# Kernel optimization log

Measured on AMD Instinct MI355X. Metric: run time of the kernel, lower is better.

## Reference

```python
import jax, jax.numpy as jnp
import numpy as np

FILTERS = [1, 3, 7, 9]
BN_EPS = 1e-5


def _conv1d(x, w, b):
    # x: [B, C, L], w: [O, I, F] (torch Conv1d layout), 'same' padding for odd F
    pad = (w.shape[-1] - 1) // 2
    y = jax.lax.conv_general_dilated(
        x, w, window_strides=(1,), padding=[(pad, pad)],
        dimension_numbers=("NCH", "OIH", "NCH"))
    return y + b[None, :, None]


def _bn_elu(x, gamma, beta):
    # BatchNorm1d in training mode: biased batch stats over (batch, length)
    m = jnp.mean(x, axis=(0, 2), keepdims=True)
    v = jnp.var(x, axis=(0, 2), keepdims=True)
    xn = (x - m) * jax.lax.rsqrt(v + BN_EPS)
    return jax.nn.elu(xn * gamma[None, :, None] + beta[None, :, None])


def setup_inputs() -> dict:
    key = jax.random.key(0)
    ks = jax.random.split(key, 32)
    b, h, l, lk, dk = 8, 8, 1024, 1024, 64
    inp = {
        "Q": jax.random.normal(ks[0], (b, h, l, dk), jnp.float32),
        "K": jax.random.normal(ks[1], (b, h, lk, dk), jnp.float32),
        "V": jax.random.normal(ks[2], (b, h, lk, dk), jnp.float32),
        "W_pq": jax.random.normal(ks[3], (1, dk), jnp.float32) * 0.1,
        "W_bq": jax.random.normal(ks[4], (dk, 1), jnp.float32) * 0.1,
        "W_bk": jax.random.normal(ks[5], (dk, 1), jnp.float32) * 0.1,
        "bn_g": jax.random.uniform(ks[6], (h,), jnp.float32, 0.5, 1.5),
        "bn_b": jax.random.normal(ks[7], (h,), jnp.float32) * 0.1,
        "attn_mask": jnp.ones((1,), dtype=bool),
    }
    for i, f in enumerate(FILTERS):
        s = 1.0 / np.sqrt(h * f)
        inp[f"cq_w{i}"] = jax.random.normal(ks[8 + i], (h, h, f), jnp.float32) * s
        inp[f"cq_b{i}"] = jax.random.normal(ks[12 + i], (h,), jnp.float32) * 0.05
        inp[f"ck_w{i}"] = jax.random.normal(ks[16 + i], (h, h, f), jnp.float32) * s
        inp[f"ck_b{i}"] = jax.random.normal(ks[20 + i], (h,), jnp.float32) * 0.05
    return inp


def reference(Q, K, V, W_pq, W_bq, W_bk,
              cq_w0, cq_b0, cq_w1, cq_b1, cq_w2, cq_b2, cq_w3, cq_b3,
              ck_w0, ck_b0, ck_w1, ck_b1, ck_w2, ck_b2, ck_w3, ck_b3,
              bn_g, bn_b, attn_mask):
    b, h, l, dk = Q.shape
    lk = K.shape[2]
    nf = len(FILTERS)
    # proj_q applied to BOTH Q and K (proj_k is dead in the original code)
    q = jnp.einsum("bhld,d->bhl", Q, W_pq[0])  # [b,h,l]
    k = jnp.einsum("bhld,d->bhl", K, W_pq[0])  # [b,h,lk]
    cq = [(cq_w0, cq_b0), (cq_w1, cq_b1), (cq_w2, cq_b2), (cq_w3, cq_b3)]
    ck = [(ck_w0, ck_b0), (ck_w1, ck_b1), (ck_w2, ck_b2), (ck_w3, ck_b3)]
    Q_l = [_bn_elu(_conv1d(q, w, bb), bn_g, bn_b) for w, bb in cq]
    K_l = [_bn_elu(_conv1d(k, w, bb), bn_g, bn_b) for w, bb in ck]
    # replicate torch.cat(dim=0) + reshape(b,h,nf*len) flat-order semantics
    Q_p = jnp.concatenate(Q_l, axis=0).reshape(b, h, nf * l)    # [b,h,4l]
    K_p = jnp.concatenate(K_l, axis=0).reshape(b, h, nf * lk)   # [b,h,4lk]
    Qt = jax.lax.top_k(Q_p, l)[0]                               # [b,h,l]
    Km = jnp.mean(K_p.reshape(b, h, nf, lk), axis=2)            # [b,h,lk]
    Kt = jax.lax.top_k(Km, lk)[0]                               # descending sort
    Qb = Qt[..., None] * W_bq[:, 0]                             # [b,h,l,dk]
    Kb = Kt[..., None] * W_bk[:, 0]                             # [b,h,lk,dk]
    scores = jnp.einsum("bhqd,bhkd->bhqk", Qb, Kb) / np.float32(np.sqrt(dk))
    attn = jax.nn.softmax(scores, axis=-1)
    context = jnp.einsum("bhqk,bhkd->bhqd", attn, V)
    return context, attn
```

## Files before the change

kernel.cpp:

```cpp
#include <hip/hip_runtime.h>
#include <hip/hip_bf16.h>
#include <math.h>

namespace {
constexpr int CONV_OFF = 131072;
constexpr int PS_OFF   = 655360;
constexpr int PSS_OFF  = 659456;

typedef short bf16x8 __attribute__((ext_vector_type(8)));
typedef float f32x4 __attribute__((ext_vector_type(4)));

union BF8 {
  bf16x8 v;
  short s[8];
};

__device__ inline float bn_elu(float v, float mean, float rstd, float g,
                               float be) {
  const float x = (v - mean) * rstd * g + be;
  return x > 0.f ? x : expm1f(x);
}

__device__ inline void cswap(float& a, float& b, bool up) {
  const float mx = fmaxf(a, b), mn = fminf(a, b);
  a = up ? mx : mn;
  b = up ? mn : mx;
}

__device__ inline void wsort1024(float v[16], int lane) {
#pragma unroll
  for (int k = 2; k <= 1024; k <<= 1) {
#pragma unroll
    for (int j = 512; j >= 16; j >>= 1) {
      if (j <= (k >> 1)) {
        const int lj = j >> 4;
        const bool up = ((lane & (k >> 4)) == 0);
        const bool keep = (up == ((lane & lj) == 0));
#pragma unroll
        for (int e = 0; e < 16; ++e) {
          const float p = __shfl_xor(v[e], lj, 64);
          v[e] = keep ? fmaxf(v[e], p) : fminf(v[e], p);
        }
      }
    }
#pragma unroll
    for (int j = 8; j >= 1; j >>= 1) {
      if (j <= (k >> 1)) {
#pragma unroll
        for (int e = 0; e < 16; ++e) {
          if ((e & j) == 0) {
            bool up;
            if (k >= 32)
              up = ((lane & (k >> 4)) == 0);
            else if (k == 16)
              up = ((lane & 1) == 0);
            else
              up = ((e & k) == 0);
            cswap(v[e], v[e ^ j], up);
          }
        }
      }
    }
  }
}

__device__ inline void wmerge1024(float v[16], int lane) {
#pragma unroll
  for (int lj = 32; lj >= 1; lj >>= 1) {
    const bool keep = ((lane & lj) == 0);
#pragma unroll
    for (int e = 0; e < 16; ++e) {
      const float p = __shfl_xor(v[e], lj, 64);
      v[e] = keep ? fmaxf(v[e], p) : fminf(v[e], p);
    }
  }
#pragma unroll
  for (int j = 8; j >= 1; j >>= 1)
#pragma unroll
    for (int e = 0; e < 16; ++e)
      if ((e & j) == 0) cswap(v[e], v[e ^ j], true);
}

template <int F>
__device__ inline void pc_filter(const float* __restrict__ xs,
                                 const float* __restrict__ wsm, float bias,
                                 float* __restrict__ outp, int grp, int ln,
                                 int lq, float& sv, float& qv) {
  constexpr int pad = (F - 1) / 2;
  sv = 0.f;
  qv = 0.f;
#pragma unroll
  for (int i = 0; i < 4; ++i) {
    const int l = ln + 32 * i;
    float acc = bias;
#pragma unroll
    for (int c = 0; c < 8; ++c) {
      const float* xrow = &xs[c * 136 + l + 4 - pad];
      const float* wrow = &wsm[(grp * 8 + c) * F];
#pragma unroll
      for (int f = 0; f < F; ++f) acc = fmaf(xrow[f], wrow[f], acc);
    }
    outp[grp * 1024 + lq * 128 + l] = acc;
    sv += acc;
    qv = fmaf(acc, acc, qv);
  }
}

__global__ __launch_bounds__(256) void projconv_kernel(
    const float* __restrict__ Q, const float* __restrict__ K,
    const float* __restrict__ Wpq,
    const float* __restrict__ wq0, const float* __restrict__ bq0,
    const float* __restrict__ wq1, const float* __restrict__ bq1,
    const float* __restrict__ wq2, const float* __restrict__ bq2,
    const float* __restrict__ wq3, const float* __restrict__ bq3,
    const float* __restrict__ wk0, const float* __restrict__ bk0,
    const float* __restrict__ wk1, const float* __restrict__ bk1,
    const float* __restrict__ wk2, const float* __restrict__ bk2,
    const float* __restrict__ wk3, const float* __restrict__ bk3,
    float* __restrict__ conv, float* __restrict__ psum,
    float* __restrict__ psumsq) {
  __shared__ float xs[8 * 136];
  __shared__ float wsh[64];
  __shared__ float wsm[1280];
  __shared__ float bsm[32];
  const int tid = threadIdx.x;
  const int blk = blockIdx.x;
  const int path = blk >> 6, bb = (blk >> 3) & 7, lq = blk & 7;
  const float* X = path == 0 ? Q : K;
  const float* w0 = path == 0 ? wq0 : wk0;
  const float* w1 = path == 0 ? wq1 : wk1;
  const float* w2 = path == 0 ? wq2 : wk2;
  const float* w3 = path == 0 ? wq3 : wk3;
  const float* b0 = path == 0 ? bq0 : bk0;
  const float* b1 = path == 0 ? bq1 : bk1;
  const float* b2 = path == 0 ? bq2 : bk2;
  const float* b3 = path == 0 ? bq3 : bk3;
  if (tid < 64) wsh[tid] = Wpq[tid];
  for (int e = tid; e < 64; e += 256) wsm[e] = w0[e];
  for (int e = tid; e < 192; e += 256) wsm[64 + e] = w1[e];
  for (int e = tid; e < 448; e += 256) wsm[256 + e] = w2[e];
  for (int e = tid; e < 576; e += 256) wsm[704 + e] = w3[e];
  if (tid < 8)
    bsm[tid] = b0[tid];
  else if (tid < 16)
    bsm[tid] = b1[tid - 8];
  else if (tid < 24)
    bsm[tid] = b2[tid - 16];
  else if (tid < 32)
    bsm[tid] = b3[tid - 24];
  __syncthreads();
  for (int w = tid; w < 1088; w += 256) {
    const int c = w / 136, p = w - c * 136;
    const int gl = lq * 128 + p - 4;
    float acc = 0.f;
    if (gl >= 0 && gl < 1024) {
      const float* src = X + ((size_t)(bb * 8 + c) * 1024 + gl) * 64;
#pragma unroll
      for (int j = 0; j < 16; ++j) {
        const float4 x4 = *(const float4*)(src + j * 4);
        acc = fmaf(x4.x, wsh[j * 4 + 0], acc);
        acc = fmaf(x4.y, wsh[j * 4 + 1], acc);
        acc = fmaf(x4.z, wsh[j * 4 + 2], acc);
        acc = fmaf(x4.w, wsh[j * 4 + 3], acc);
      }
    }
    xs[c * 136 + p] = acc;
  }
  __syncthreads();
  const int grp = tid >> 5, ln = tid & 31;
  float sv, qv;
#define PC_DO(fi, F, WOFF)                                                   \
  pc_filter<F>(xs, wsm + WOFF, bsm[fi * 8 + grp],                            \
               conv + (size_t)((path * 4 + fi) * 8 + bb) * 8192, grp, ln,    \
               lq, sv, qv);                                                  \
  _Pragma("unroll") for (int m = 16; m >= 1; m >>= 1) {                      \
    sv += __shfl_xor(sv, m, 64);                                             \
    qv += __shfl_xor(qv, m, 64);                                             \
  }                                                                          \
  if (ln == 0) {                                                             \
    psum[((path * 4 + fi) * 8 + grp) * 64 + bb * 8 + lq] = sv;               \
    psumsq[((path * 4 + fi) * 8 + grp) * 64 + bb * 8 + lq] = qv;             \
  }
  PC_DO(0, 1, 0)
  PC_DO(1, 3, 64)
  PC_DO(2, 7, 256)
  PC_DO(3, 9, 704)
#undef PC_DO
}

__global__ __launch_bounds__(256, 4) void attn6_kernel(
    const float* __restrict__ V, const float* __restrict__ conv,
    const float* __restrict__ psum, const float* __restrict__ psumsq,
    const float* __restrict__ bng, const float* __restrict__ bnb,
    const float* __restrict__ Wbq, const float* __restrict__ Wbk,
    float* __restrict__ ctx, float* __restrict__ attn) {
  __shared__ float Kts[1024];
  __shared__ float sq[64], mq[64], rz[64];
  __shared__ short Vhi[2][8 * 64 * 8];
  __shared__ short Vlo[2][8 * 64 * 8];
  float* s1 = (float*)&Vhi[0][0];
  float* s2 = (float*)&Vlo[0][0];
  const int tid = threadIdx.x;
  const int b = blockIdx.x;
  const int bh = ((b & 7) << 3) | ((b >> 3) & 7);
  const int qt = b >> 6;
  const int qbase = qt * 64;
  const int wv = tid >> 6, l = tid & 63;
  float cval;
  {
    float d = Wbq[l] * Wbk[l];
#pragma unroll
    for (int mm = 32; mm >= 1; mm >>= 1) d += __shfl_xor(d, mm, 64);
    cval = d * 0.125f;
  }
  const int hp = bh & 7, fib = bh >> 4;
  const int bbb = ((bh >> 3) & 1) * 4 + (hp >> 1);
  float v[16];
  {
    const int hh = (hp & 1) * 4 + wv;
    const int ch = fib * 8 + hh;
    float sval = 0.f;
    if (l < 2) {
      const float* src = (l == 0) ? psum : psumsq;
#pragma unroll
      for (int i = 0; i < 64; ++i) sval += src[ch * 64 + i];
    }
    const float mean = __shfl(sval, 0, 64) * (1.f / 8192.f);
    const float msq = __shfl(sval, 1, 64) * (1.f / 8192.f);
    const float rstd = rsqrtf(fmaxf(msq - mean * mean, 0.f) + 1e-5f);
    const float g = bng[hh], be = bnb[hh];
    const float* base = conv + (size_t)(fib * 8 + bbb) * 8192 + hh * 1024;
#pragma unroll
    for (int j = 0; j < 4; ++j) {
      const float4 x = *(const float4*)&base[l * 16 + j * 4];
      v[j * 4 + 0] = bn_elu(x.x, mean, rstd, g, be);
      v[j * 4 + 1] = bn_elu(x.y, mean, rstd, g, be);
      v[j * 4 + 2] = bn_elu(x.z, mean, rstd, g, be);
      v[j * 4 + 3] = bn_elu(x.w, mean, rstd, g, be);
    }
    wsort1024(v, l);
  }
  __syncthreads();
  if (wv == 1)
#pragma unroll
    for (int e = 0; e < 16; ++e) s1[l * 16 + e] = v[e];
  if (wv == 3)
#pragma unroll
    for (int e = 0; e < 16; ++e) s2[l * 16 + e] = v[e];
  __syncthreads();
  if (wv == 0) {
#pragma unroll
    for (int e = 0; e < 16; ++e) v[e] = fmaxf(v[e], s1[1023 - (l * 16 + e)]);
    wmerge1024(v, l);
  } else if (wv == 2) {
#pragma unroll
    for (int e = 0; e < 16; ++e) v[e] = fmaxf(v[e], s2[1023 - (l * 16 + e)]);
    wmerge1024(v, l);
  } else if (wv == 1) {
    const int chk = 32 + fib * 8 + (hp & 1) * 4;
    float sval = 0.f;
    if (l < 8) {
      const float* src = (l < 4) ? psum : psumsq;
      const int ch = chk + (l & 3);
#pragma unroll
      for (int i = 0; i < 64; ++i) sval += src[ch * 64 + i];
    }
    float cm[4], cr[4];
#pragma unroll
    for (int j = 0; j < 4; ++j) {
      const float mean = __shfl(sval, j, 64) * (1.f / 8192.f);
      const float msq = __shfl(sval, j + 4, 64) * (1.f / 8192.f);
      cm[j] = mean;
      cr[j] = rsqrtf(fmaxf(msq - mean * mean, 0.f) + 1e-5f);
    }
#pragma unroll
    for (int e = 0; e < 16; ++e) v[e] = 0.f;
#pragma unroll
    for (int j = 0; j < 4; ++j) {
      const int hh = (hp & 1) * 4 + j;
      const float g = bng[hh], be = bnb[hh];
      const float* base = conv + (size_t)(4 + fib) * 64 * 1024 +
                          (size_t)bbb * 8192 + hh * 1024;
#pragma unroll
      for (int jj = 0; jj < 4; ++jj) {
        const float4 x = *(const float4*)&base[l * 16 + jj * 4];
        v[jj * 4 + 0] += bn_elu(x.x, cm[j], cr[j], g, be);
        v[jj * 4 + 1] += bn_elu(x.y, cm[j], cr[j], g, be);
        v[jj * 4 + 2] += bn_elu(x.z, cm[j], cr[j], g, be);
        v[jj * 4 + 3] += bn_elu(x.w, cm[j], cr[j], g, be);
      }
    }
#pragma unroll
    for (int e = 0; e < 16; ++e) v[e] *= 0.25f;
    wsort1024(v, l);
  }
  __syncthreads();
  if (wv == 2)
#pragma unroll
    for (int e = 0; e < 16; ++e) s2[l * 16 + e] = v[e];
  if (wv == 1)
#pragma unroll
    for (int e = 0; e < 16; ++e) Kts[l * 16 + e] = v[e];
  __syncthreads();
  if (wv == 0) {
#pragma unroll
    for (int e = 0; e < 16; ++e) v[e] = fmaxf(v[e], s2[1023 - (l * 16 + e)]);
    wmerge1024(v, l);
    const int d = l - qt * 4;
    if (d >= 0 && d < 4) {
      const float kHi = Kts[0], kLo = Kts[1023];
#pragma unroll
      for (int e = 0; e < 16; ++e) {
        const float s = cval * v[e];
        sq[d * 16 + e] = s;
        mq[d * 16 + e] = fmaxf(s * kHi, s * kLo);
      }
    }
  }
  __syncthreads();
  {
    const int row = tid >> 2, qtr = tid & 3;
    const float s = sq[row], m = mq[row];
    float z = 0.f;
    const int k0 = qtr * 256;
    for (int k = 0; k < 256; ++k) z += __expf(fmaf(s, Kts[k0 + k], -m));
    z += __shfl_xor(z, 1, 64);
    z += __shfl_xor(z, 2, 64);
    if (qtr == 0) rz[row] = 1.f / z;
  }
  __syncthreads();

  const int l15 = l & 15, l4 = l >> 4;
  const int q = wv * 16 + l15;
  const float s = sq[q], m = mq[q], r = rz[q];
  f32x4 acc[4];
#pragma unroll
  for (int dt = 0; dt < 4; ++dt) acc[dt] = (f32x4){0.f, 0.f, 0.f, 0.f};

  const float* Vb = V + (size_t)bh * 65536;
  float* arow = attn + ((size_t)bh << 20) + (size_t)qbase * 1024;
  const int dV = tid & 63, kqV = tid >> 6;

  for (int ch = 0; ch < 16; ++ch) {
    const int kc = ch * 64;
    const int buf = ch & 1;
    float vreg[2][8];
#pragma unroll
    for (int g = 0; g < 2; ++g) {
      const int ko = kqV + g * 4;
      const float* vs = Vb + (size_t)(kc + ko * 8) * 64 + dV;
#pragma unroll
      for (int i = 0; i < 8; ++i) vreg[g][i] = vs[i * 64];
    }
    bf16x8 ahi[2], alo[2];
#pragma unroll
    for (int ks = 0; ks < 2; ++ks) {
      const int kb = kc + ks * 32 + l4 * 8;
      const float4 kv0 = *(const float4*)&Kts[kb];
      const float4 kv1 = *(const float4*)&Kts[kb + 4];
      float e[8];
      e[0] = __expf(fmaf(s, kv0.x, -m)) * r;
      e[1] = __expf(fmaf(s, kv0.y, -m)) * r;
      e[2] = __expf(fmaf(s, kv0.z, -m)) * r;
      e[3] = __expf(fmaf(s, kv0.w, -m)) * r;
      e[4] = __expf(fmaf(s, kv1.x, -m)) * r;
      e[5] = __expf(fmaf(s, kv1.y, -m)) * r;
      e[6] = __expf(fmaf(s, kv1.z, -m)) * r;
      e[7] = __expf(fmaf(s, kv1.w, -m)) * r;
      float* ag = arow + (size_t)q * 1024 + kb;
      *(float4*)ag = make_float4(e[0], e[1], e[2], e[3]);
      *(float4*)(ag + 4) = make_float4(e[4], e[5], e[6], e[7]);
      BF8 H, L;
#pragma unroll
      for (int i = 0; i < 8; ++i) {
        const __hip_bfloat16 hb = __float2bfloat16(e[i]);
        H.s[i] = __bfloat16_as_short(hb);
        L.s[i] =
            __bfloat16_as_short(__float2bfloat16(e[i] - __bfloat162float(hb)));
      }
      ahi[ks] = H.v;
      alo[ks] = L.v;
    }
#pragma unroll
    for (int g = 0; g < 2; ++g) {
      const int ko = kqV + g * 4;
      BF8 H, L;
#pragma unroll
      for (int i = 0; i < 8; ++i) {
        const float f = vreg[g][i];
        const __hip_bfloat16 hb = __float2bfloat16(f);
        H.s[i] = __bfloat16_as_short(hb);
        L.s[i] =
            __bfloat16_as_short(__float2bfloat16(f - __bfloat162float(hb)));
      }
      *(bf16x8*)&Vhi[buf][(ko * 64 + dV) * 8] = H.v;
      *(bf16x8*)&Vlo[buf][(ko * 64 + dV) * 8] = L.v;
    }
    __syncthreads();
#pragma unroll
    for (int ks = 0; ks < 2; ++ks) {
      const int ko = ks * 4 + l4;
#pragma unroll
      for (int dt = 0; dt < 4; ++dt) {
        const bf16x8 bhv =
            *(const bf16x8*)&Vhi[buf][(ko * 64 + dt * 16 + l15) * 8];
        const bf16x8 blv =
            *(const bf16x8*)&Vlo[buf][(ko * 64 + dt * 16 + l15) * 8];
        acc[dt] = __builtin_amdgcn_mfma_f32_16x16x32_bf16(ahi[ks], bhv,
                                                          acc[dt], 0, 0, 0);
        acc[dt] = __builtin_amdgcn_mfma_f32_16x16x32_bf16(ahi[ks], blv,
                                                          acc[dt], 0, 0, 0);
        acc[dt] = __builtin_amdgcn_mfma_f32_16x16x32_bf16(alo[ks], bhv,
                                                          acc[dt], 0, 0, 0);
      }
    }
  }
  float* cb = ctx + ((size_t)bh * 1024 + qbase + wv * 16 + l4 * 4) * 64 + l15;
#pragma unroll
  for (int dt = 0; dt < 4; ++dt)
#pragma unroll
    for (int rr = 0; rr < 4; ++rr) cb[(size_t)rr * 64 + dt * 16] = acc[dt][rr];
}

}

extern "C" void kernel_launch(void* const* d_in, const int* in_sizes, int n_in,
                              void* d_out, int out_size, void* d_ws,
                              size_t ws_size, hipStream_t stream) {
  const float* Q = (const float*)d_in[0];
  const float* K = (const float*)d_in[1];
  const float* V = (const float*)d_in[2];
  const float* Wpq = (const float*)d_in[3];
  const float* Wbq = (const float*)d_in[4];
  const float* Wbk = (const float*)d_in[5];
  const float* bng = (const float*)d_in[6];
  const float* bnb = (const float*)d_in[7];
  const float* cqw[4] = {(const float*)d_in[9], (const float*)d_in[13],
                         (const float*)d_in[17], (const float*)d_in[21]};
  const float* cqb[4] = {(const float*)d_in[10], (const float*)d_in[14],
                         (const float*)d_in[18], (const float*)d_in[22]};
  const float* ckw[4] = {(const float*)d_in[11], (const float*)d_in[15],
                         (const float*)d_in[19], (const float*)d_in[23]};
  const float* ckb[4] = {(const float*)d_in[12], (const float*)d_in[16],
                         (const float*)d_in[20], (const float*)d_in[24]};

  float* ws = (float*)d_ws;
  float* conv = ws + CONV_OFF;
  float* psum = ws + PS_OFF;
  float* psumsq = ws + PSS_OFF;
  float* ctx = (float*)d_out;
  float* attn = ctx + (size_t)8 * 8 * 1024 * 64;

  projconv_kernel<<<128, 256, 0, stream>>>(
      Q, K, Wpq, cqw[0], cqb[0], cqw[1], cqb[1], cqw[2], cqb[2], cqw[3],
      cqb[3], ckw[0], ckb[0], ckw[1], ckb[1], ckw[2], ckb[2], ckw[3], ckb[3],
      conv, psum, psumsq);
  attn6_kernel<<<1024, 256, 0, stream>>>(V, conv, psum, psumsq, bng, bnb, Wbq,
                                         Wbk, ctx, attn);
}
```

Measured before the change: 128.4 us.

## Hoist per-row sort/merge out of attention into a dedicated kernel

The attention kernel previously re-ran the BN+ELU, bitonic sorts and merges for a whole (b,h) row in every one of its 1024 blocks, so each row's sort was repeated once per query tile. A new 80-block kernel sorts each Q row (64 blocks) and each averaged K row (16 blocks, one row per wave) exactly once and writes Qt/Kt to workspace. The attention kernel then just loads the sorted Kt into shared memory and its 64 Qt values. This removes the redundant sort work. In exchange it adds a kernel launch, a global round-trip for the sorted rows, and a small low-occupancy kernel on the critical path.

```diff
diff --git a/kernel.cpp b/kernel.cpp
--- a/kernel.cpp
+++ b/kernel.cpp
@@ -6,6 +6,8 @@
 constexpr int CONV_OFF = 131072;
 constexpr int PS_OFF   = 655360;
 constexpr int PSS_OFF  = 659456;
+constexpr int QT_OFF   = 663552;
+constexpr int KT_OFF   = 729088;
 
 typedef short bf16x8 __attribute__((ext_vector_type(8)));
 typedef float f32x4 __attribute__((ext_vector_type(4)));
@@ -188,37 +190,22 @@
 #undef PC_DO
 }
 
-__global__ __launch_bounds__(256, 4) void attn6_kernel(
-    const float* __restrict__ V, const float* __restrict__ conv,
-    const float* __restrict__ psum, const float* __restrict__ psumsq,
-    const float* __restrict__ bng, const float* __restrict__ bnb,
-    const float* __restrict__ Wbq, const float* __restrict__ Wbk,
-    float* __restrict__ ctx, float* __restrict__ attn) {
-  __shared__ float Kts[1024];
-  __shared__ float sq[64], mq[64], rz[64];
-  __shared__ short Vhi[2][8 * 64 * 8];
-  __shared__ short Vlo[2][8 * 64 * 8];
-  float* s1 = (float*)&Vhi[0][0];
-  float* s2 = (float*)&Vlo[0][0];
-  const int tid = threadIdx.x;
-  const int b = blockIdx.x;
-  const int bh = ((b & 7) << 3) | ((b >> 3) & 7);
-  const int qt = b >> 6;
-  const int qbase = qt * 64;
+__global__ __launch_bounds__(256) void sortmerge2_kernel(
+    const float* __restrict__ conv, const float* __restrict__ psum,
+    const float* __restrict__ psumsq, const float* __restrict__ bng,
+    const float* __restrict__ bnb, float* __restrict__ Qt,
+    float* __restrict__ Kt) {
+  __shared__ float s1[1024];
+  __shared__ float s2[1024];
+  const int tid = threadIdx.x, blk = blockIdx.x;
   const int wv = tid >> 6, l = tid & 63;
-  float cval;
-  {
-    float d = Wbq[l] * Wbk[l];
-#pragma unroll
-    for (int mm = 32; mm >= 1; mm >>= 1) d += __shfl_xor(d, mm, 64);
-    cval = d * 0.125f;
-  }
-  const int hp = bh & 7, fib = bh >> 4;
-  const int bbb = ((bh >> 3) & 1) * 4 + (hp >> 1);
   float v[16];
-  {
+  if (blk < 64) {
+    const int row = blk;
+    const int hp = row & 7, fi = row >> 4;
+    const int bb = ((row >> 3) & 1) * 4 + (hp >> 1);
     const int hh = (hp & 1) * 4 + wv;
-    const int ch = fib * 8 + hh;
+    const int ch = fi * 8 + hh;
     float sval = 0.f;
     if (l < 2) {
       const float* src = (l == 0) ? psum : psumsq;
@@ -229,7 +216,7 @@
     const float msq = __shfl(sval, 1, 64) * (1.f / 8192.f);
     const float rstd = rsqrtf(fmaxf(msq - mean * mean, 0.f) + 1e-5f);
     const float g = bng[hh], be = bnb[hh];
-    const float* base = conv + (size_t)(fib * 8 + bbb) * 8192 + hh * 1024;
+    const float* base = conv + (size_t)(fi * 8 + bb) * 8192 + hh * 1024;
 #pragma unroll
     for (int j = 0; j < 4; ++j) {
       const float4 x = *(const float4*)&base[l * 16 + j * 4];
@@ -239,25 +226,40 @@
       v[j * 4 + 3] = bn_elu(x.w, mean, rstd, g, be);
     }
     wsort1024(v, l);
-  }
-  __syncthreads();
-  if (wv == 1)
-#pragma unroll
-    for (int e = 0; e < 16; ++e) s1[l * 16 + e] = v[e];
-  if (wv == 3)
-#pragma unroll
-    for (int e = 0; e < 16; ++e) s2[l * 16 + e] = v[e];
-  __syncthreads();
-  if (wv == 0) {
-#pragma unroll
-    for (int e = 0; e < 16; ++e) v[e] = fmaxf(v[e], s1[1023 - (l * 16 + e)]);
-    wmerge1024(v, l);
-  } else if (wv == 2) {
-#pragma unroll
-    for (int e = 0; e < 16; ++e) v[e] = fmaxf(v[e], s2[1023 - (l * 16 + e)]);
-    wmerge1024(v, l);
-  } else if (wv == 1) {
-    const int chk = 32 + fib * 8 + (hp & 1) * 4;
+    if (wv == 1)
+#pragma unroll
+      for (int e = 0; e < 16; ++e) s1[l * 16 + e] = v[e];
+    if (wv == 3)
+#pragma unroll
+      for (int e = 0; e < 16; ++e) s2[l * 16 + e] = v[e];
+    __syncthreads();
+    if (wv == 0) {
+#pragma unroll
+      for (int e = 0; e < 16; ++e) v[e] = fmaxf(v[e], s1[1023 - (l * 16 + e)]);
+      wmerge1024(v, l);
+    } else if (wv == 2) {
+#pragma unroll
+      for (int e = 0; e < 16; ++e) v[e] = fmaxf(v[e], s2[1023 - (l * 16 + e)]);
+      wmerge1024(v, l);
+#pragma unroll
+      for (int e = 0; e < 16; ++e) s2[l * 16 + e] = v[e];
+    }
+    __syncthreads();
+    if (wv == 0) {
+#pragma unroll
+      for (int e = 0; e < 16; ++e) v[e] = fmaxf(v[e], s2[1023 - (l * 16 + e)]);
+      wmerge1024(v, l);
+      float* qd = Qt + (size_t)row * 1024 + l * 16;
+#pragma unroll
+      for (int j = 0; j < 4; ++j)
+        *(float4*)&qd[j * 4] =
+            make_float4(v[j * 4], v[j * 4 + 1], v[j * 4 + 2], v[j * 4 + 3]);
+    }
+  } else {
+    const int row = (blk - 64) * 4 + wv;
+    const int hp = row & 7, fi = row >> 4;
+    const int bb = ((row >> 3) & 1) * 4 + (hp >> 1);
+    const int chk = 32 + fi * 8 + (hp & 1) * 4;
     float sval = 0.f;
     if (l < 8) {
       const float* src = (l < 4) ? psum : psumsq;
@@ -279,8 +281,8 @@
     for (int j = 0; j < 4; ++j) {
       const int hh = (hp & 1) * 4 + j;
       const float g = bng[hh], be = bnb[hh];
-      const float* base = conv + (size_t)(4 + fib) * 64 * 1024 +
-                          (size_t)bbb * 8192 + hh * 1024;
+      const float* base =
+          conv + (size_t)(4 + fi) * 64 * 1024 + (size_t)bb * 8192 + hh * 1024;
 #pragma unroll
       for (int jj = 0; jj < 4; ++jj) {
         const float4 x = *(const float4*)&base[l * 16 + jj * 4];
@@ -293,29 +295,43 @@
 #pragma unroll
     for (int e = 0; e < 16; ++e) v[e] *= 0.25f;
     wsort1024(v, l);
-  }
-  __syncthreads();
-  if (wv == 2)
-#pragma unroll
-    for (int e = 0; e < 16; ++e) s2[l * 16 + e] = v[e];
-  if (wv == 1)
-#pragma unroll
-    for (int e = 0; e < 16; ++e) Kts[l * 16 + e] = v[e];
-  __syncthreads();
-  if (wv == 0) {
-#pragma unroll
-    for (int e = 0; e < 16; ++e) v[e] = fmaxf(v[e], s2[1023 - (l * 16 + e)]);
-    wmerge1024(v, l);
-    const int d = l - qt * 4;
-    if (d >= 0 && d < 4) {
-      const float kHi = Kts[0], kLo = Kts[1023];
-#pragma unroll
-      for (int e = 0; e < 16; ++e) {
-        const float s = cval * v[e];
-        sq[d * 16 + e] = s;
-        mq[d * 16 + e] = fmaxf(s * kHi, s * kLo);
-      }
-    }
+    float* kd = Kt + (size_t)row * 1024 + l * 16;
+#pragma unroll
+    for (int j = 0; j < 4; ++j)
+      *(float4*)&kd[j * 4] =
+          make_float4(v[j * 4], v[j * 4 + 1], v[j * 4 + 2], v[j * 4 + 3]);
+  }
+}
+
+__global__ __launch_bounds__(256, 4) void attn5_kernel(
+    const float* __restrict__ V, const float* __restrict__ Qt,
+    const float* __restrict__ Kt, const float* __restrict__ Wbq,
+    const float* __restrict__ Wbk, float* __restrict__ ctx,
+    float* __restrict__ attn) {
+  __shared__ float Kts[1024];
+  __shared__ float sq[64], mq[64], rz[64];
+  __shared__ short Vhi[2][8 * 64 * 8];
+  __shared__ short Vlo[2][8 * 64 * 8];
+  const int tid = threadIdx.x;
+  const int b = blockIdx.x;
+  const int bh = ((b & 7) << 3) | ((b >> 3) & 7);
+  const int qt = b >> 6;
+  const int qbase = qt * 64;
+  const int lane0 = tid & 63;
+  float cval;
+  {
+    float d = Wbq[lane0] * Wbk[lane0];
+#pragma unroll
+    for (int mm = 32; mm >= 1; mm >>= 1) d += __shfl_xor(d, mm, 64);
+    cval = d * 0.125f;
+  }
+  const float* Ktg = Kt + (size_t)bh * 1024;
+  for (int t = tid; t < 1024; t += 256) Kts[t] = Ktg[t];
+  const float kHi = Ktg[0], kLo = Ktg[1023];
+  if (tid < 64) {
+    const float s = cval * Qt[(size_t)bh * 1024 + qbase + tid];
+    sq[tid] = s;
+    mq[tid] = fmaxf(s * kHi, s * kLo);
   }
   __syncthreads();
   {
@@ -330,6 +346,7 @@
   }
   __syncthreads();
 
+  const int wv = tid >> 6, l = tid & 63;
   const int l15 = l & 15, l4 = l >> 4;
   const int q = wv * 16 + l15;
   const float s = sq[q], m = mq[q], r = rz[q];
@@ -448,6 +465,8 @@
   float* conv = ws + CONV_OFF;
   float* psum = ws + PS_OFF;
   float* psumsq = ws + PSS_OFF;
+  float* Qtp = ws + QT_OFF;
+  float* Ktp = ws + KT_OFF;
   float* ctx = (float*)d_out;
   float* attn = ctx + (size_t)8 * 8 * 1024 * 64;
 
@@ -455,6 +474,7 @@
       Q, K, Wpq, cqw[0], cqb[0], cqw[1], cqb[1], cqw[2], cqb[2], cqw[3],
       cqb[3], ckw[0], ckb[0], ckw[1], ckb[1], ckw[2], ckb[2], ckw[3], ckb[3],
       conv, psum, psumsq);
-  attn6_kernel<<<1024, 256, 0, stream>>>(V, conv, psum, psumsq, bng, bnb, Wbq,
-                                         Wbk, ctx, attn);
-}
+  sortmerge2_kernel<<<80, 256, 0, stream>>>(conv, psum, psumsq, bng, bnb, Qtp,
+                                            Ktp);
+  attn5_kernel<<<1024, 256, 0, stream>>>(V, Qtp, Ktp, Wbq, Wbk, ctx, attn);
+}
```

After: 116.8 us. 1.1x faster.
